# Optimization experiments

Hardware: AMD Instinct MI355X
Metric: run time of the kernel (lower is better)

The kernel has to match this reference:

```python
import jax, jax.numpy as jnp
import numpy as np

VOCAB = 100000
EMBED = 128

def setup_inputs() -> dict:
    key = jax.random.key(0)
    k1, k2, k3 = jax.random.split(key, 3)
    x = jax.random.randint(k1, (4096, 200), 0, VOCAB, dtype=jnp.int64)
    # torch Linear(vocab, embed): weight [embed, vocab], bias [embed]
    W = jax.random.normal(k2, (EMBED, VOCAB), dtype=jnp.float32) * (1.0 / np.sqrt(VOCAB))
    b = jax.random.normal(k3, (EMBED,), dtype=jnp.float32) * 0.01
    return {"x": x, "W": W, "b": b}

def reference(x, W, b):
    # one_hot(x) @ W.T + b  ==  gather rows of W.T at x, then add bias.
    # Same math as the original scatter+Linear, expressed as a row-gather.
    y = jnp.take(W.T, x, axis=0)  # [B, T, EMBED]
    return y + b
```

## Files before the change

kernel.cpp:

```cpp
#include <hip/hip_runtime.h>


#define EMB 128

typedef float fx4 __attribute__((ext_vector_type(4)));

__global__ void transpose_bias_kernel(const float* __restrict__ W,
                                      const float* __restrict__ bias,
                                      float* __restrict__ Wt, int V) {
    __shared__ float lds[64 * 129];
    const int v0 = blockIdx.x * 64;
    const int t  = threadIdx.x;

    #pragma unroll 8
    for (int j = t; j < 128 * 64; j += 256) {
        const int e    = j >> 6;
        const int vloc = j & 63;
        const int v    = v0 + vloc;
        float val = 0.0f;
        if (v < V) val = W[(size_t)e * V + v];
        lds[vloc * 129 + e] = val;
    }
    __syncthreads();

    #pragma unroll 8
    for (int j = t; j < 64 * 128; j += 256) {
        const int vloc = j >> 7;
        const int e    = j & 127;
        const int v    = v0 + vloc;
        if (v < V) Wt[(size_t)v * EMB + e] = lds[vloc * 129 + e] + bias[e];
    }
}

__global__ void gather_rows_kernel(const int* __restrict__ idx,
                                   const float* __restrict__ Wt,
                                   float* __restrict__ out, int ntok) {
    const int t = threadIdx.x;
    const int q = t & 31;
    const int g = t >> 5;
    const int ntiles = (ntok + 63) >> 6;

    for (int tile = blockIdx.x; tile < ntiles; tile += gridDim.x) {
        const int tok0 = tile << 6;
        if (tok0 + 64 <= ntok) {
            int rows[8];
            #pragma unroll
            for (int p = 0; p < 8; ++p)
                rows[p] = idx[tok0 + g + (p << 3)];

            fx4 v[8];
            #pragma unroll
            for (int p = 0; p < 8; ++p)
                v[p] = ((const fx4*)(Wt + ((size_t)rows[p] << 7)))[q];

            #pragma unroll
            for (int p = 0; p < 8; ++p)
                __builtin_nontemporal_store(
                    v[p], (fx4*)(out + ((size_t)(tok0 + g + (p << 3)) << 7)) + q);
        } else {
            #pragma unroll
            for (int p = 0; p < 8; ++p) {
                const int tok = tok0 + g + (p << 3);
                if (tok < ntok) {
                    const int row = idx[tok];
                    fx4 v = ((const fx4*)(Wt + ((size_t)row << 7)))[q];
                    __builtin_nontemporal_store(
                        v, (fx4*)(out + ((size_t)tok << 7)) + q);
                }
            }
        }
    }
}

__global__ void gather_direct_kernel(const int* __restrict__ idx,
                                     const float* __restrict__ W,
                                     const float* __restrict__ bias,
                                     float* __restrict__ out, int ntok, int V) {
    const long long total  = (long long)ntok * EMB;
    const long long stride = (long long)gridDim.x * blockDim.x;
    for (long long i = (long long)blockIdx.x * blockDim.x + threadIdx.x;
         i < total; i += stride) {
        const int token = (int)(i >> 7);
        const int e     = (int)(i & (EMB - 1));
        out[i] = W[(size_t)e * V + idx[token]] + bias[e];
    }
}

extern "C" void kernel_launch(void* const* d_in, const int* in_sizes, int n_in,
                              void* d_out, int out_size, void* d_ws, size_t ws_size,
                              hipStream_t stream) {
    const int*   x = (const int*)d_in[0];
    const float* W = (const float*)d_in[1];
    const float* b = (const float*)d_in[2];
    float* out = (float*)d_out;

    const int ntok = in_sizes[0];
    const int V    = in_sizes[1] / EMB;

    const size_t need = (size_t)V * EMB * sizeof(float);
    if (ws_size >= need) {
        float* Wt = (float*)d_ws;
        const int tblocks = (V + 63) / 64;
        transpose_bias_kernel<<<tblocks, 256, 0, stream>>>(W, b, Wt, V);
        gather_rows_kernel<<<2560, 256, 0, stream>>>(x, Wt, out, ntok);
    } else {
        gather_direct_kernel<<<2048, 256, 0, stream>>>(x, W, b, out, ntok, V);
    }
}
```

Baseline: 519.6 us.

## Deepen gather to 16 rows per thread with software-prefetched indices

The gather kernel now handles 128-token tiles, so each thread issues 16 independent row loads instead of 8. It prefetches the next tile's indices while the current tile's rows are loaded and stored. The grid is halved to 1280 blocks, and the transpose kernel reads W with nontemporal loads. The aim is more memory-level parallelism and hiding index-load latency, at the cost of higher register pressure and fewer blocks.

```diff
diff --git a/kernel.cpp b/kernel.cpp
--- a/kernel.cpp
+++ b/kernel.cpp
@@ -18,7 +18,7 @@
         const int vloc = j & 63;
         const int v    = v0 + vloc;
         float val = 0.0f;
-        if (v < V) val = W[(size_t)e * V + v];
+        if (v < V) val = __builtin_nontemporal_load(&W[(size_t)e * V + v]);
         lds[vloc * 129 + e] = val;
     }
     __syncthreads();
@@ -32,43 +32,61 @@
     }
 }
 
-__global__ void gather_rows_kernel(const int* __restrict__ idx,
-                                   const float* __restrict__ Wt,
-                                   float* __restrict__ out, int ntok) {
+__global__ __launch_bounds__(256) void gather_rows_deep(
+        const int* __restrict__ idx, const float* __restrict__ Wt,
+        float* __restrict__ out, int ntok) {
     const int t = threadIdx.x;
     const int q = t & 31;
     const int g = t >> 5;
-    const int ntiles = (ntok + 63) >> 6;
+    const int niter  = (ntok + 127) >> 7;
+    const int stride = gridDim.x;
 
-    for (int tile = blockIdx.x; tile < ntiles; tile += gridDim.x) {
-        const int tok0 = tile << 6;
-        if (tok0 + 64 <= ntok) {
-            int rows[8];
+    int it = blockIdx.x;
+    if (it >= niter) return;
+
+    int rows[16];
+    {
+        const int tok0 = it << 7;
+        #pragma unroll
+        for (int p = 0; p < 16; ++p) {
+            const int tok = tok0 + g + (p << 3);
+            rows[p] = (tok < ntok) ? idx[tok] : 0;
+        }
+    }
+
+    while (it < niter) {
+        const int it_n = it + stride;
+
+        int rows_n[16];
+        if (it_n < niter) {
+            const int tok0n = it_n << 7;
             #pragma unroll
-            for (int p = 0; p < 8; ++p)
-                rows[p] = idx[tok0 + g + (p << 3)];
-
-            fx4 v[8];
-            #pragma unroll
-            for (int p = 0; p < 8; ++p)
-                v[p] = ((const fx4*)(Wt + ((size_t)rows[p] << 7)))[q];
-
-            #pragma unroll
-            for (int p = 0; p < 8; ++p)
-                __builtin_nontemporal_store(
-                    v[p], (fx4*)(out + ((size_t)(tok0 + g + (p << 3)) << 7)) + q);
+            for (int p = 0; p < 16; ++p) {
+                const int tok = tok0n + g + (p << 3);
+                rows_n[p] = (tok < ntok) ? idx[tok] : 0;
+            }
         } else {
             #pragma unroll
-            for (int p = 0; p < 8; ++p) {
-                const int tok = tok0 + g + (p << 3);
-                if (tok < ntok) {
-                    const int row = idx[tok];
-                    fx4 v = ((const fx4*)(Wt + ((size_t)row << 7)))[q];
-                    __builtin_nontemporal_store(
-                        v, (fx4*)(out + ((size_t)tok << 7)) + q);
-                }
-            }
+            for (int p = 0; p < 16; ++p) rows_n[p] = 0;
         }
+
+        fx4 v[16];
+        #pragma unroll
+        for (int p = 0; p < 16; ++p)
+            v[p] = ((const fx4*)(Wt + ((size_t)rows[p] << 7)))[q];
+
+        const int tok0 = it << 7;
+        #pragma unroll
+        for (int p = 0; p < 16; ++p) {
+            const int tok = tok0 + g + (p << 3);
+            if (tok < ntok)
+                __builtin_nontemporal_store(
+                    v[p], (fx4*)(out + ((size_t)tok << 7)) + q);
+        }
+
+        #pragma unroll
+        for (int p = 0; p < 16; ++p) rows[p] = rows_n[p];
+        it = it_n;
     }
 }
 
@@ -102,7 +120,7 @@
         float* Wt = (float*)d_ws;
         const int tblocks = (V + 63) / 64;
         transpose_bias_kernel<<<tblocks, 256, 0, stream>>>(W, b, Wt, V);
-        gather_rows_kernel<<<2560, 256, 0, stream>>>(x, Wt, out, ntok);
+        gather_rows_deep<<<1280, 256, 0, stream>>>(x, Wt, out, ntok);
     } else {
         gather_direct_kernel<<<2048, 256, 0, stream>>>(x, W, b, out, ntok, V);
     }
```

Result: no change. 518.1 us (-0.3%).
